# Kernel optimization log

Hardware: AMD Instinct MI355X
Metric: run time of the kernel (lower is better)

Reference implementation:

```python
import jax, jax.numpy as jnp
import numpy as np

N, E, F_IN, H, L, G, C = 50000, 640000, 128, 128, 3, 256, 10
NEG_SLOPE = 0.2  # PyG GATConv default leaky_relu slope


def setup_inputs() -> dict:
    key = jax.random.key(0)
    ks = jax.random.split(key, 10)
    x = jax.random.normal(ks[0], (N, F_IN), jnp.float32)
    edge_index = jax.random.randint(ks[1], (2, E), 0, N, dtype=jnp.int32)
    # sorted graph ids covering all G graphs (global_max_pool segments)
    batch = (jnp.arange(N, dtype=jnp.int32) * G) // N
    s = 1.0 / np.sqrt(H)
    # 3 GAT layers all map 128->128 (F_IN == H), so stack their params
    Wc = jax.random.normal(ks[2], (L, F_IN, H), jnp.float32) * s
    a_src = jax.random.normal(ks[3], (L, H), jnp.float32) * s
    a_dst = jax.random.normal(ks[4], (L, H), jnp.float32) * s
    bc = jnp.zeros((L, H), jnp.float32)
    W1 = jax.random.normal(ks[5], (H, H), jnp.float32) * s
    b1 = jnp.zeros((H,), jnp.float32)
    W2 = jax.random.normal(ks[6], (H, C), jnp.float32) * s
    b2 = jnp.zeros((C,), jnp.float32)
    return dict(x=x, edge_index=edge_index, batch=batch, Wc=Wc, a_src=a_src,
                a_dst=a_dst, bc=bc, W1=W1, b1=b1, W2=W2, b2=b2)


def _gat_layer(h_in, W, a_s, a_d, b, src, dst):
    h = h_in @ W                                   # [N, H]
    e_s = (h * a_s).sum(-1)                        # [N] source term
    e_d = (h * a_d).sum(-1)                        # [N] target term
    e = jax.nn.leaky_relu(e_s[src] + e_d[dst], NEG_SLOPE)  # [E']
    # softmax over incoming edges of each target node
    m = jax.ops.segment_max(e, dst, num_segments=N)
    w = jnp.exp(e - m[dst])
    z = jax.ops.segment_sum(w, dst, num_segments=N)
    alpha = w / (z[dst] + 1e-16)
    out = jax.ops.segment_sum(alpha[:, None] * h[src], dst, num_segments=N)
    return out + b


def reference(x, edge_index, batch, Wc, a_src, a_dst, bc, W1, b1, W2, b2):
    loops = jnp.arange(N, dtype=edge_index.dtype)  # GATConv adds self-loops
    src = jnp.concatenate([edge_index[0], loops])
    dst = jnp.concatenate([edge_index[1], loops])
    h = x
    for l in range(L):
        h = jax.nn.relu(_gat_layer(h, Wc[l], a_src[l], a_dst[l], bc[l], src, dst))
    g = jax.ops.segment_max(h, batch, num_segments=G)  # global_max_pool [G, H]
    g = jax.nn.relu(g @ W1 + b1)
    logits = g @ W2 + b2
    return jax.nn.log_softmax(logits, axis=-1)
```

## Files before the change

### kernel.cpp

```cpp
#include <hip/hip_runtime.h>
#include <hip/hip_fp16.h>
#include <math.h>

#define N_ 50000
#define E_ 640000
#define H_ 128
#define L_ 3
#define G_ 256
#define C_ 10
#define NEG_SLOPE 0.2f

#define ABLK ((N_ + 3) / 4)
#define MAXDEG 64
#define CURPAD 16

typedef _Float16 half8 __attribute__((ext_vector_type(8)));
typedef float f32x4 __attribute__((ext_vector_type(4)));

__device__ __forceinline__ float leaky(float x) { return x > 0.f ? x : NEG_SLOPE * x; }
__device__ __forceinline__ int pi_out(int p) { return ((p & 7) << 4) + (p >> 3); }

__global__ void zero_i32(int* __restrict__ p, int n) {
    int i = blockIdx.x * blockDim.x + threadIdx.x;
    if (i < n) p[i] = 0;
}

__global__ __launch_bounds__(256) void fill_prep(const int* __restrict__ src,
                                                 const int* __restrict__ dst,
                                                 int* __restrict__ cur_pad,
                                                 int* __restrict__ col_slots,
                                                 const float* __restrict__ Wc,
                                                 const float* __restrict__ a_src,
                                                 const float* __restrict__ a_dst,
                                                 const float* __restrict__ bc,
                                                 __half* __restrict__ Wt,
                                                 float* __restrict__ bcp) {
    if (blockIdx.x < L_) {
        int l = blockIdx.x;
        const float* W = Wc + l * 16384;
        __half* T = Wt + (size_t)l * 144 * 128;
        int t = threadIdx.x;
        for (int e = t; e < 16384; e += 256) {
            int n = e >> 7, p = e & 127;
            int ks = (l == 0) ? p : pi_out(p);
            T[n * 128 + p] = __float2half(W[ks * 128 + n]);
        }
        if (t < 128) {
            int p = t;
            int ks = (l == 0) ? p : pi_out(p);
            const float* as = a_src + l * 128;
            const float* ad = a_dst + l * 128;
            float s = 0.f, d = 0.f;
#pragma unroll 8
            for (int n = 0; n < 128; n++) {
                float w = W[ks * 128 + n];
                s += w * as[n];
                d += w * ad[n];
            }
            T[128 * 128 + p] = __float2half(s);
            T[129 * 128 + p] = __float2half(d);
            bcp[l * 128 + p] = bc[l * 128 + pi_out(p)];
        } else {
            int kk = t - 128;
            for (int r = 130; r < 144; r++) T[r * 128 + kk] = __float2half(0.f);
        }
    } else {
        int i = (blockIdx.x - L_) * 256 + threadIdx.x;
        if (i < E_) {
            int d = dst[i];
            int p = atomicAdd(&cur_pad[d * CURPAD], 1);
            if (p < MAXDEG) col_slots[d * MAXDEG + p] = src[i];
        }
    }
}

template <bool FP16IN>
__global__ __launch_bounds__(256) void gemm_mfma(const void* __restrict__ Av,
                                                 const __half* __restrict__ Wt,
                                                 __half* __restrict__ h16,
                                                 float* __restrict__ es,
                                                 float* __restrict__ ed) {
    __shared__ __half Asw[64 * 128];
    __shared__ __half Bsw[144 * 128];
    int tid = threadIdx.x;
    int brow = blockIdx.x * 64;

    {
        int r = tid >> 2;
        int q = tid & 3;
        int grow = brow + r;
        if (FP16IN) {
            const __half* Ah = (const __half*)Av;
            float4 vv[4];
            if (grow < N_) {
                const float4* p = (const float4*)(Ah + (size_t)grow * 128 + q * 32);
#pragma unroll
                for (int s = 0; s < 4; s++) vv[s] = p[s];
            } else {
                float4 zz = make_float4(0.f, 0.f, 0.f, 0.f);
#pragma unroll
                for (int s = 0; s < 4; s++) vv[s] = zz;
            }
#pragma unroll
            for (int s = 0; s < 4; s++) {
                int kbyte = q * 64 + s * 16;
                int addr = r * 256 + (kbyte ^ ((r & 7) << 4));
                *(float4*)((char*)Asw + addr) = vv[s];
            }
        } else {
            const float* A = (const float*)Av;
            int kc = q * 32;
            float v[32];
            if (grow < N_) {
                const float4* p = (const float4*)(A + (size_t)grow * 128 + kc);
#pragma unroll
                for (int s = 0; s < 8; s++) {
                    float4 f = p[s];
                    v[s * 4] = f.x; v[s * 4 + 1] = f.y; v[s * 4 + 2] = f.z; v[s * 4 + 3] = f.w;
                }
            } else {
#pragma unroll
                for (int s = 0; s < 32; s++) v[s] = 0.f;
            }
#pragma unroll
            for (int s = 0; s < 4; s++) {
                half8 h;
#pragma unroll
                for (int j = 0; j < 8; j++) h[j] = (_Float16)v[s * 8 + j];
                int kbyte = kc * 2 + s * 16;
                int addr = r * 256 + (kbyte ^ ((r & 7) << 4));
                *(half8*)((char*)Asw + addr) = h;
            }
        }
    }
    {
        const float4* src = (const float4*)Wt;
#pragma unroll
        for (int i = 0; i < 9; i++) {
            int c = tid + i * 256;
            int o = c * 16;
            int n = o >> 8;
            float4 val = src[c];
            int addr = n * 256 + ((o & 255) ^ ((n & 7) << 4));
            *(float4*)((char*)Bsw + addr) = val;
        }
    }
    __syncthreads();

    int w = tid >> 6, l = tid & 63;
    int lrow = l & 15, lk = l >> 4;
    f32x4 acc[9];
#pragma unroll
    for (int t = 0; t < 9; t++) acc[t] = (f32x4)0.f;
#pragma unroll
    for (int kk = 0; kk < 4; kk++) {
        int kbyte = kk * 64 + lk * 16;
        int arow = w * 16 + lrow;
        half8 af = *(const half8*)((const char*)Asw + arow * 256 + (kbyte ^ ((arow & 7) << 4)));
#pragma unroll
        for (int t = 0; t < 9; t++) {
            int n = t * 16 + lrow;
            half8 bf = *(const half8*)((const char*)Bsw + n * 256 + (kbyte ^ ((n & 7) << 4)));
            acc[t] = __builtin_amdgcn_mfma_f32_16x16x32_f16(af, bf, acc[t], 0, 0, 0);
        }
    }

    int row0 = brow + w * 16 + lk * 4;
#pragma unroll
    for (int r = 0; r < 4; r++) {
        int grow = row0 + r;
        if (grow < N_) {
            half8 hv;
#pragma unroll
            for (int t = 0; t < 8; t++) hv[t] = (_Float16)acc[t][r];
            *(half8*)(h16 + (size_t)grow * 128 + lrow * 8) = hv;
            if (lrow == 0) es[grow] = acc[8][r];
            else if (lrow == 1) ed[grow] = acc[8][r];
        }
    }
}

__global__ __launch_bounds__(256) void gat_aggregate(const __half* __restrict__ h16,
                                                     const float* __restrict__ es,
                                                     const float* __restrict__ ed,
                                                     const int* __restrict__ cur_pad,
                                                     const int* __restrict__ col_slots,
                                                     const float* __restrict__ biasp,
                                                     __half* __restrict__ hout) {
    __shared__ int   lds_s[4][64];
    __shared__ float lds_w[4][64];
    int wv = threadIdx.x >> 6;
    int lane = threadIdx.x & 63;
    int node = blockIdx.x * 4 + wv;
    if (node >= N_) return;
    int deg = min(cur_pad[node * CURPAD], MAXDEG);
    float edn = ed[node];
    float es_self = es[node];

    int c0 = 0;
    float w0 = 0.f;
    if (lane < deg) {
        c0 = col_slots[node * MAXDEG + lane];
        w0 = __expf(fminf(leaky(es[c0] + edn), 30.f));
    }
    float zl = w0;
    lds_s[wv][lane] = c0;
    lds_w[wv][lane] = w0;

    int eg = lane >> 4;
    int fl = lane & 15;

    float acc[8] = {0.f, 0.f, 0.f, 0.f, 0.f, 0.f, 0.f, 0.f};
#pragma unroll 4
    for (int j = eg; j < deg; j += 4) {
        int s = lds_s[wv][j];
        float a = lds_w[wv][j];
        union { float4 f4; __half2 h2[4]; } u;
        u.f4 = *(const float4*)(h16 + (size_t)s * 128 + fl * 8);
#pragma unroll
        for (int q = 0; q < 4; q++) {
            float2 fv = __half22float2(u.h2[q]);
            acc[2 * q]     += a * fv.x;
            acc[2 * q + 1] += a * fv.y;
        }
    }

#pragma unroll
    for (int q = 0; q < 8; q++) {
        acc[q] += __shfl_xor(acc[q], 16);
        acc[q] += __shfl_xor(acc[q], 32);
    }
#pragma unroll
    for (int o = 32; o; o >>= 1) zl += __shfl_xor(zl, o);
    float ws = __expf(fminf(leaky(es_self + edn), 30.f));
    float inv = 1.0f / (zl + ws + 1e-16f);

    if (eg == 0) {
        union { float4 f4; __half2 h2[4]; } su;
        su.f4 = *(const float4*)(h16 + (size_t)node * 128 + fl * 8);
        const float4* bp = (const float4*)(biasp + fl * 8);
        float4 b0 = bp[0], b1 = bp[1];
        float bq[8] = {b0.x, b0.y, b0.z, b0.w, b1.x, b1.y, b1.z, b1.w};
        union { float4 f4; __half2 h2[4]; } ou;
#pragma unroll
        for (int q = 0; q < 4; q++) {
            float2 sv = __half22float2(su.h2[q]);
            float v0 = fmaxf((acc[2 * q]     + ws * sv.x) * inv + bq[2 * q],     0.f);
            float v1 = fmaxf((acc[2 * q + 1] + ws * sv.y) * inv + bq[2 * q + 1], 0.f);
            ou.h2[q] = __floats2half2_rn(v0, v1);
        }
        *(float4*)(hout + (size_t)node * 128 + fl * 8) = ou.f4;
    }
}

__device__ __forceinline__ int lower_bound_batch(const int* __restrict__ batch, int val) {
    int lo = 0, hi = N_;
    while (lo < hi) {
        int mid = (lo + hi) >> 1;
        if (batch[mid] < val) lo = mid + 1;
        else hi = mid;
    }
    return lo;
}

__global__ __launch_bounds__(512) void pool_head(const __half* __restrict__ h16,
                                                 const int* __restrict__ batch,
                                                 const float* __restrict__ W1,
                                                 const float* __restrict__ b1,
                                                 const float* __restrict__ W2,
                                                 const float* __restrict__ b2,
                                                 float* __restrict__ out) {
    int g = blockIdx.x;
    int t = threadIdx.x;
    __shared__ float red[8][128];
    __shared__ float gs[128], gp[128], lg[C_], lse;

    int s = lower_bound_batch(batch, g);
    int e = lower_bound_batch(batch, g + 1);
    int fs = t & 15;
    int rg = t >> 4;
    float m[8] = {0.f, 0.f, 0.f, 0.f, 0.f, 0.f, 0.f, 0.f};
    for (int i = s + rg; i < e; i += 32) {
        union { float4 f4; __half2 h2[4]; } u;
        u.f4 = *(const float4*)(h16 + (size_t)i * 128 + fs * 8);
#pragma unroll
        for (int q = 0; q < 4; q++) {
            float2 fv = __half22float2(u.h2[q]);
            m[2 * q]     = fmaxf(m[2 * q],     fv.x);
            m[2 * q + 1] = fmaxf(m[2 * q + 1], fv.y);
        }
    }
#pragma unroll
    for (int q = 0; q < 8; q++) {
        m[q] = fmaxf(m[q], __shfl_xor(m[q], 16));
        m[q] = fmaxf(m[q], __shfl_xor(m[q], 32));
    }
    int wid = t >> 6;
    if ((t & 48) == 0) {
#pragma unroll
        for (int q = 0; q < 8; q++) red[wid][fs * 8 + q] = m[q];
    }
    __syncthreads();
    if (t < 128) {
        float mm = red[0][t];
#pragma unroll
        for (int w = 1; w < 8; w++) mm = fmaxf(mm, red[w][t]);
        gs[t] = mm;
    }
    __syncthreads();

    if (t < 128) {
        float acc = b1[t];
#pragma unroll 8
        for (int k = 0; k < 128; k++) {
            int f = pi_out(k);
            acc += gs[k] * W1[f * 128 + t];
        }
        gp[t] = fmaxf(acc, 0.f);
    }
    __syncthreads();
    if (t < C_) {
        float a2 = b2[t];
#pragma unroll 8
        for (int k = 0; k < 128; k++) a2 += gp[k] * W2[k * C_ + t];
        lg[t] = a2;
    }
    __syncthreads();
    if (t == 0) {
        float mm = lg[0];
#pragma unroll
        for (int i = 1; i < C_; i++) mm = fmaxf(mm, lg[i]);
        float ss = 0.f;
#pragma unroll
        for (int i = 0; i < C_; i++) ss += expf(lg[i] - mm);
        lse = mm + logf(ss);
    }
    __syncthreads();
    if (t < C_) out[g * C_ + t] = lg[t] - lse;
}

extern "C" void kernel_launch(void* const* d_in, const int* in_sizes, int n_in,
                              void* d_out, int out_size, void* d_ws, size_t ws_size,
                              hipStream_t stream) {
    const float* x     = (const float*)d_in[0];
    const int*   eidx  = (const int*)d_in[1];
    const int*   batch = (const int*)d_in[2];
    const float* Wc    = (const float*)d_in[3];
    const float* a_src = (const float*)d_in[4];
    const float* a_dst = (const float*)d_in[5];
    const float* bc    = (const float*)d_in[6];
    const float* W1    = (const float*)d_in[7];
    const float* b1    = (const float*)d_in[8];
    const float* W2    = (const float*)d_in[9];
    const float* b2    = (const float*)d_in[10];
    float* out = (float*)d_out;

    const int* srcs = eidx;
    const int* dsts = eidx + E_;

    __half* hG16  = (__half*)d_ws;
    __half* hB16  = hG16 + (size_t)N_ * 128;
    float*  es    = (float*)(hB16 + (size_t)N_ * 128);
    float*  ed    = es + N_;
    float*  bcp   = ed + N_;
    __half* Wt    = (__half*)(bcp + 3 * 128);
    int*    cur_pad   = (int*)(Wt + (size_t)3 * 144 * 128);
    int*    col_slots = cur_pad + (size_t)CURPAD * N_;

    zero_i32<<<(CURPAD * N_ + 1023) / 1024, 1024, 0, stream>>>(cur_pad, CURPAD * N_);
    fill_prep<<<L_ + (E_ + 255) / 256, 256, 0, stream>>>(srcs, dsts, cur_pad, col_slots,
                                                         Wc, a_src, a_dst, bc, Wt, bcp);

    int gblk = (N_ + 63) / 64;
    gemm_mfma<false><<<gblk, 256, 0, stream>>>(x, Wt, hG16, es, ed);
    gat_aggregate<<<ABLK, 256, 0, stream>>>(hG16, es, ed, cur_pad, col_slots, bcp, hB16);
    for (int l = 1; l < L_; ++l) {
        gemm_mfma<true><<<gblk, 256, 0, stream>>>(
            hB16, Wt + (size_t)l * 144 * 128, hG16, es, ed);
        gat_aggregate<<<ABLK, 256, 0, stream>>>(hG16, es, ed, cur_pad, col_slots,
                                                bcp + l * 128, hB16);
    }

    pool_head<<<G_, 512, 0, stream>>>(hB16, batch, W1, b1, W2, b2, out);
}
```

Measured before the change: 194.1 us.

## Fuse edge bucketing with layer-0 GEMM and drop padded degree counters

Removes the padded (stride-16) per-node counter array and its large zero kernel, folding the zeroing into a small kernel that also preps layer-0 weights. The edge-bucketing atomics, the first-layer MFMA GEMM and the prep of layers 1-2 now run as disjoint block ranges of one launch, so the irregular scatter can overlap with the GEMM. Each fill thread now handles four edges. Unpadded counters put neighbouring nodes' atomics on the same cache lines, which may add contention.

New measurement: 203.6 us. 4.9% more time.

```diff
diff --git a/kernel.cpp b/kernel.cpp
--- a/kernel.cpp
+++ b/kernel.cpp
@@ -12,7 +12,8 @@
 
 #define ABLK ((N_ + 3) / 4)
 #define MAXDEG 64
-#define CURPAD 16
+#define FILL_BLKS 625
+#define GEMM_BLKS ((N_ + 63) / 64)
 
 typedef _Float16 half8 __attribute__((ext_vector_type(8)));
 typedef float f32x4 __attribute__((ext_vector_type(4)));
@@ -20,70 +21,66 @@
 __device__ __forceinline__ float leaky(float x) { return x > 0.f ? x : NEG_SLOPE * x; }
 __device__ __forceinline__ int pi_out(int p) { return ((p & 7) << 4) + (p >> 3); }
 
-__global__ void zero_i32(int* __restrict__ p, int n) {
-    int i = blockIdx.x * blockDim.x + threadIdx.x;
-    if (i < n) p[i] = 0;
-}
-
-__global__ __launch_bounds__(256) void fill_prep(const int* __restrict__ src,
-                                                 const int* __restrict__ dst,
-                                                 int* __restrict__ cur_pad,
-                                                 int* __restrict__ col_slots,
-                                                 const float* __restrict__ Wc,
-                                                 const float* __restrict__ a_src,
-                                                 const float* __restrict__ a_dst,
-                                                 const float* __restrict__ bc,
-                                                 __half* __restrict__ Wt,
-                                                 float* __restrict__ bcp) {
-    if (blockIdx.x < L_) {
-        int l = blockIdx.x;
-        const float* W = Wc + l * 16384;
-        __half* T = Wt + (size_t)l * 144 * 128;
-        int t = threadIdx.x;
-        for (int e = t; e < 16384; e += 256) {
-            int n = e >> 7, p = e & 127;
-            int ks = (l == 0) ? p : pi_out(p);
-            T[n * 128 + p] = __float2half(W[ks * 128 + n]);
-        }
-        if (t < 128) {
-            int p = t;
-            int ks = (l == 0) ? p : pi_out(p);
-            const float* as = a_src + l * 128;
-            const float* ad = a_dst + l * 128;
-            float s = 0.f, d = 0.f;
+__device__ __forceinline__ void prep_layer(int l, const float* __restrict__ Wc,
+                                           const float* __restrict__ a_src,
+                                           const float* __restrict__ a_dst,
+                                           const float* __restrict__ bc,
+                                           __half* __restrict__ Wt,
+                                           float* __restrict__ bcp) {
+    const float* W = Wc + l * 16384;
+    __half* T = Wt + (size_t)l * 144 * 128;
+    int t = threadIdx.x;
+    for (int e = t; e < 16384; e += 256) {
+        int n = e >> 7, p = e & 127;
+        int ks = (l == 0) ? p : pi_out(p);
+        T[n * 128 + p] = __float2half(W[ks * 128 + n]);
+    }
+    if (t < 128) {
+        int p = t;
+        int ks = (l == 0) ? p : pi_out(p);
+        const float* as = a_src + l * 128;
+        const float* ad = a_dst + l * 128;
+        float s = 0.f, d = 0.f;
 #pragma unroll 8
-            for (int n = 0; n < 128; n++) {
-                float w = W[ks * 128 + n];
-                s += w * as[n];
-                d += w * ad[n];
-            }
-            T[128 * 128 + p] = __float2half(s);
-            T[129 * 128 + p] = __float2half(d);
-            bcp[l * 128 + p] = bc[l * 128 + pi_out(p)];
-        } else {
-            int kk = t - 128;
-            for (int r = 130; r < 144; r++) T[r * 128 + kk] = __float2half(0.f);
-        }
+        for (int n = 0; n < 128; n++) {
+            float w = W[ks * 128 + n];
+            s += w * as[n];
+            d += w * ad[n];
+        }
+        T[128 * 128 + p] = __float2half(s);
+        T[129 * 128 + p] = __float2half(d);
+        bcp[l * 128 + p] = bc[l * 128 + pi_out(p)];
     } else {
-        int i = (blockIdx.x - L_) * 256 + threadIdx.x;
-        if (i < E_) {
-            int d = dst[i];
-            int p = atomicAdd(&cur_pad[d * CURPAD], 1);
-            if (p < MAXDEG) col_slots[d * MAXDEG + p] = src[i];
-        }
+        int kk = t - 128;
+        for (int r = 130; r < 144; r++) T[r * 128 + kk] = __float2half(0.f);
+    }
+}
+
+__global__ __launch_bounds__(256) void zero_prep0(int* __restrict__ cur,
+                                                  const float* __restrict__ Wc,
+                                                  const float* __restrict__ a_src,
+                                                  const float* __restrict__ a_dst,
+                                                  const float* __restrict__ bc,
+                                                  __half* __restrict__ Wt,
+                                                  float* __restrict__ bcp) {
+    if (blockIdx.x == 0) {
+        prep_layer(0, Wc, a_src, a_dst, bc, Wt, bcp);
+    } else {
+        int i = (blockIdx.x - 1) * 256 + threadIdx.x;
+        if (i < N_) cur[i] = 0;
     }
 }
 
 template <bool FP16IN>
-__global__ __launch_bounds__(256) void gemm_mfma(const void* __restrict__ Av,
-                                                 const __half* __restrict__ Wt,
-                                                 __half* __restrict__ h16,
-                                                 float* __restrict__ es,
-                                                 float* __restrict__ ed) {
-    __shared__ __half Asw[64 * 128];
-    __shared__ __half Bsw[144 * 128];
+__device__ __forceinline__ void gemm_body(int bid, const void* __restrict__ Av,
+                                          const __half* __restrict__ Wt,
+                                          __half* __restrict__ h16,
+                                          float* __restrict__ es,
+                                          float* __restrict__ ed,
+                                          __half* __restrict__ Asw,
+                                          __half* __restrict__ Bsw) {
     int tid = threadIdx.x;
-    int brow = blockIdx.x * 64;
+    int brow = bid * 64;
 
     {
         int r = tid >> 2;
@@ -180,10 +177,58 @@
     }
 }
 
+__global__ __launch_bounds__(256) void mega0(const int* __restrict__ src,
+                                             const int* __restrict__ dst,
+                                             int* __restrict__ cur,
+                                             int* __restrict__ col_slots,
+                                             const float* __restrict__ x,
+                                             const float* __restrict__ Wc,
+                                             const float* __restrict__ a_src,
+                                             const float* __restrict__ a_dst,
+                                             const float* __restrict__ bc,
+                                             __half* __restrict__ Wt,
+                                             float* __restrict__ bcp,
+                                             __half* __restrict__ h16,
+                                             float* __restrict__ es,
+                                             float* __restrict__ ed) {
+    __shared__ __half Asw[64 * 128];
+    __shared__ __half Bsw[144 * 128];
+    int bx = blockIdx.x;
+    if (bx < FILL_BLKS) {
+        int b = bx * 1024 + threadIdx.x;
+        int e0 = b, e1 = b + 256, e2 = b + 512, e3 = b + 768;
+        int d0 = dst[e0], d1 = dst[e1], d2 = dst[e2], d3 = dst[e3];
+        int s0 = src[e0], s1 = src[e1], s2 = src[e2], s3 = src[e3];
+        int p0 = atomicAdd(&cur[d0], 1);
+        int p1 = atomicAdd(&cur[d1], 1);
+        int p2 = atomicAdd(&cur[d2], 1);
+        int p3 = atomicAdd(&cur[d3], 1);
+        if (p0 < MAXDEG) col_slots[d0 * MAXDEG + p0] = s0;
+        if (p1 < MAXDEG) col_slots[d1 * MAXDEG + p1] = s1;
+        if (p2 < MAXDEG) col_slots[d2 * MAXDEG + p2] = s2;
+        if (p3 < MAXDEG) col_slots[d3 * MAXDEG + p3] = s3;
+    } else if (bx < FILL_BLKS + GEMM_BLKS) {
+        gemm_body<false>(bx - FILL_BLKS, x, Wt, h16, es, ed, Asw, Bsw);
+    } else {
+        prep_layer(bx - (FILL_BLKS + GEMM_BLKS) + 1, Wc, a_src, a_dst, bc, Wt, bcp);
+    }
+}
+
+template <bool FP16IN>
+__global__ __launch_bounds__(256) void gemm_mfma(const void* __restrict__ Av,
+                                                 const __half* __restrict__ Wt,
+                                                 __half* __restrict__ h16,
+                                                 float* __restrict__ es,
+                                                 float* __restrict__ ed) {
+    __shared__ __half Asw[64 * 128];
+    __shared__ __half Bsw[144 * 128];
+    gemm_body<FP16IN>(blockIdx.x, Av, Wt, h16, es, ed, Asw, Bsw);
+}
+
 __global__ __launch_bounds__(256) void gat_aggregate(const __half* __restrict__ h16,
                                                      const float* __restrict__ es,
                                                      const float* __restrict__ ed,
-                                                     const int* __restrict__ cur_pad,
+                                                     const int* __restrict__ cur,
                                                      const int* __restrict__ col_slots,
                                                      const float* __restrict__ biasp,
                                                      __half* __restrict__ hout) {
@@ -193,7 +238,7 @@
     int lane = threadIdx.x & 63;
     int node = blockIdx.x * 4 + wv;
     if (node >= N_) return;
-    int deg = min(cur_pad[node * CURPAD], MAXDEG);
+    int deg = min(cur[node], MAXDEG);
     float edn = ed[node];
     float es_self = es[node];
 
@@ -364,20 +409,19 @@
     float*  ed    = es + N_;
     float*  bcp   = ed + N_;
     __half* Wt    = (__half*)(bcp + 3 * 128);
-    int*    cur_pad   = (int*)(Wt + (size_t)3 * 144 * 128);
-    int*    col_slots = cur_pad + (size_t)CURPAD * N_;
-
-    zero_i32<<<(CURPAD * N_ + 1023) / 1024, 1024, 0, stream>>>(cur_pad, CURPAD * N_);
-    fill_prep<<<L_ + (E_ + 255) / 256, 256, 0, stream>>>(srcs, dsts, cur_pad, col_slots,
-                                                         Wc, a_src, a_dst, bc, Wt, bcp);
-
-    int gblk = (N_ + 63) / 64;
-    gemm_mfma<false><<<gblk, 256, 0, stream>>>(x, Wt, hG16, es, ed);
-    gat_aggregate<<<ABLK, 256, 0, stream>>>(hG16, es, ed, cur_pad, col_slots, bcp, hB16);
+    int*    cur       = (int*)(Wt + (size_t)3 * 144 * 128);
+    int*    col_slots = cur + N_;
+
+    zero_prep0<<<1 + (N_ + 255) / 256, 256, 0, stream>>>(cur, Wc, a_src, a_dst, bc, Wt, bcp);
+
+    mega0<<<FILL_BLKS + GEMM_BLKS + 2, 256, 0, stream>>>(
+        srcs, dsts, cur, col_slots, x, Wc, a_src, a_dst, bc, Wt, bcp, hG16, es, ed);
+
+    gat_aggregate<<<ABLK, 256, 0, stream>>>(hG16, es, ed, cur, col_slots, bcp, hB16);
     for (int l = 1; l < L_; ++l) {
-        gemm_mfma<true><<<gblk, 256, 0, stream>>>(
+        gemm_mfma<true><<<GEMM_BLKS, 256, 0, stream>>>(
             hB16, Wt + (size_t)l * 144 * 128, hG16, es, ed);
-        gat_aggregate<<<ABLK, 256, 0, stream>>>(hG16, es, ed, cur_pad, col_slots,
+        gat_aggregate<<<ABLK, 256, 0, stream>>>(hG16, es, ed, cur, col_slots,
                                                 bcp + l * 128, hB16);
     }
 
```
